# Kernel tuning notes

Measured on AMD Instinct MI355X. Metric: run time of the kernel, lower is better.

## Reference

```python
import jax, jax.numpy as jnp
import numpy as np

N, E, IN_CH, OUT_CH = 8192, 4096, 256, 256
EPS = 1e-06


def setup_inputs() -> dict:
    key = jax.random.key(0)
    k1, k2, k3, k4 = jax.random.split(key, 4)
    x = jax.random.normal(k1, (N, IN_CH), dtype=jnp.float32)
    H = jax.random.uniform(k2, (N, E), dtype=jnp.float32)
    # nn.Linear(in_ch, out_ch): weight [out_ch, in_ch], bias [out_ch]
    lim = 1.0 / np.sqrt(IN_CH)
    W = jax.random.uniform(k3, (OUT_CH, IN_CH), dtype=jnp.float32, minval=-lim, maxval=lim)
    b = jax.random.uniform(k4, (OUT_CH,), dtype=jnp.float32, minval=-lim, maxval=lim)
    return {"x": x, "H": H, "W": W, "b": b}


def reference(x, H, W, b):
    # A = Dv^{-1/2} H De^{-1} H^T Dv^{-1/2}; out = (A x) W^T + b
    d_e = H.sum(axis=0)                      # [E] hyperedge degrees
    d_v = H.sum(axis=1)                      # [N] node degrees
    de_inv = 1.0 / (d_e + EPS)               # [E]
    dv_is = (d_v + EPS) ** -0.5              # [N]
    # Diagonal matmuls expressed as row/col scaling (same math, no NxN/ExE diag GEMMs)
    xs = dv_is[:, None] * x                  # Dv^{-1/2} x            [N, C]
    t = de_inv[:, None] * (H.T @ xs)         # De^{-1} H^T (...)      [E, C]
    out = dv_is[:, None] * (H @ t)           # Dv^{-1/2} H (...)      [N, C]
    return out @ W.T + b
```

## Files before the change

kernel.cpp:

```cpp
#include <hip/hip_runtime.h>

#define NNODE 8192
#define NEDGE 4096
#define NCH   256
#define EPSV  1e-6f

typedef float  f32x4  __attribute__((ext_vector_type(4)));
typedef short  bf16x8 __attribute__((ext_vector_type(8)));
typedef unsigned short u16;
typedef unsigned int   u32;

static __device__ __forceinline__ u16 f2bf(float f) {
  union { float f; u32 u; } c; c.f = f;
  return (u16)((c.u + 0x7FFFu + ((c.u >> 16) & 1u)) >> 16);
}

static __device__ __forceinline__ void gload16(const u16* g, u16* l) {
  __builtin_amdgcn_global_load_lds((const __attribute__((address_space(1))) void*)g,
                                   (__attribute__((address_space(3))) void*)l,
                                   16, 0, 0);
}

static __device__ __forceinline__ uint4 pack8(const float4& a, const float4& c) {
  uint4 v;
  v.x = (u32)f2bf(a.x) | ((u32)f2bf(a.y) << 16);
  v.y = (u32)f2bf(a.z) | ((u32)f2bf(a.w) << 16);
  v.z = (u32)f2bf(c.x) | ((u32)f2bf(c.y) << 16);
  v.w = (u32)f2bf(c.z) | ((u32)f2bf(c.w) << 16);
  return v;
}

__global__ __launch_bounds__(256) void prep_h(const float* __restrict__ H,
                                              u16* __restrict__ HbT,
                                              float* __restrict__ d_v,
                                              float* __restrict__ d_e) {
  __shared__ float T[64][68];
  __shared__ float csp[16][68];
  __shared__ float rsum[64];
  const int t = threadIdx.x, a = t >> 4, b = t & 15;
  const int r0 = blockIdx.x * 64, c0 = blockIdx.y * 64;

  float4 v[4];
  #pragma unroll
  for (int i = 0; i < 4; ++i)
    v[i] = *(const float4*)&H[(size_t)(r0 + 4 * a + i) * NEDGE + c0 + 4 * b];

  #pragma unroll
  for (int i = 0; i < 4; ++i) {
    float rp = v[i].x + v[i].y + v[i].z + v[i].w;
    rp += __shfl_xor(rp, 1); rp += __shfl_xor(rp, 2);
    rp += __shfl_xor(rp, 4); rp += __shfl_xor(rp, 8);
    if (b == 0) rsum[4 * a + i] = rp;
  }
  csp[a][4 * b + 0] = v[0].x + v[1].x + v[2].x + v[3].x;
  csp[a][4 * b + 1] = v[0].y + v[1].y + v[2].y + v[3].y;
  csp[a][4 * b + 2] = v[0].z + v[1].z + v[2].z + v[3].z;
  csp[a][4 * b + 3] = v[0].w + v[1].w + v[2].w + v[3].w;

  {
    float4 w0 = {v[0].x, v[1].x, v[2].x, v[3].x};
    float4 w1 = {v[0].y, v[1].y, v[2].y, v[3].y};
    float4 w2 = {v[0].z, v[1].z, v[2].z, v[3].z};
    float4 w3 = {v[0].w, v[1].w, v[2].w, v[3].w};
    *(float4*)&T[4 * b + 0][4 * a] = w0;
    *(float4*)&T[4 * b + 1][4 * a] = w1;
    *(float4*)&T[4 * b + 2][4 * a] = w2;
    *(float4*)&T[4 * b + 3][4 * a] = w3;
  }
  __syncthreads();

  #pragma unroll
  for (int s = 0; s < 2; ++s) {
    const int idx = t + 256 * s;
    const int c = idx >> 3, g = idx & 7;
    const float4 p0 = *(const float4*)&T[c][8 * g];
    const float4 p1 = *(const float4*)&T[c][8 * g + 4];
    *(uint4*)&HbT[(size_t)(c0 + c) * NNODE + r0 + 8 * g] = pack8(p0, p1);
  }
  if (t < 64) {
    float s = 0.f;
    #pragma unroll
    for (int r = 0; r < 16; ++r) s += csp[r][t];
    atomicAdd(&d_e[c0 + t], s);
    atomicAdd(&d_v[r0 + t], rsum[t]);
  }
}

__global__ __launch_bounds__(256) void prep_x(const float* __restrict__ x,
                                              const float* __restrict__ d_v,
                                              u16* __restrict__ xsT) {
  __shared__ float T[64][68];
  const int t = threadIdx.x, a = t >> 4, b = t & 15;
  const int r0 = blockIdx.x * 64, c0 = blockIdx.y * 64;

  float4 v[4];
  #pragma unroll
  for (int i = 0; i < 4; ++i) {
    const int n = r0 + 4 * a + i;
    const float s = rsqrtf(d_v[n] + EPSV);
    float4 w = *(const float4*)&x[(size_t)n * NCH + c0 + 4 * b];
    w.x *= s; w.y *= s; w.z *= s; w.w *= s;
    v[i] = w;
  }
  {
    float4 w0 = {v[0].x, v[1].x, v[2].x, v[3].x};
    float4 w1 = {v[0].y, v[1].y, v[2].y, v[3].y};
    float4 w2 = {v[0].z, v[1].z, v[2].z, v[3].z};
    float4 w3 = {v[0].w, v[1].w, v[2].w, v[3].w};
    *(float4*)&T[4 * b + 0][4 * a] = w0;
    *(float4*)&T[4 * b + 1][4 * a] = w1;
    *(float4*)&T[4 * b + 2][4 * a] = w2;
    *(float4*)&T[4 * b + 3][4 * a] = w3;
  }
  __syncthreads();
  #pragma unroll
  for (int s = 0; s < 2; ++s) {
    const int idx = t + 256 * s;
    const int c = idx >> 3, g = idx & 7;
    const float4 p0 = *(const float4*)&T[c][8 * g];
    const float4 p1 = *(const float4*)&T[c][8 * g + 4];
    *(uint4*)&xsT[(size_t)(c0 + c) * NNODE + r0 + 8 * g] = pack8(p0, p1);
  }
}

__global__ __launch_bounds__(256) void prep_w(const float* __restrict__ W,
                                              u16* __restrict__ Wb) {
  const int i = (blockIdx.x * 256 + threadIdx.x) * 8;
  const float4 a = *(const float4*)&W[i];
  const float4 b = *(const float4*)&W[i + 4];
  *(uint4*)&Wb[i] = pack8(a, b);
}

__global__ __launch_bounds__(256) void init_out(const float* __restrict__ b,
                                                float* __restrict__ out) {
  const int i = (blockIdx.x * 256 + threadIdx.x) * 4;
  const float4 bb = *(const float4*)&b[i & 255];
  *(float4*)&out[i] = bb;
}

template <int ROWS, int NT>
static __device__ __forceinline__ void stage_gl(const u16* __restrict__ base,
                                                int row0, int K, int kt,
                                                u16* lds, int tid) {
  const int w = tid >> 6, l = tid & 63;
  #pragma unroll
  for (int i = 0; i < (ROWS * 8) / NT; ++i) {
    const int slot = i * NT + w * 64 + l;
    const int row = slot >> 3, ch = slot & 7;
    const int sch = ch ^ (row & 7);
    gload16(base + (size_t)(row0 + row) * K + kt + sch * 8,
            lds + (size_t)(i * NT + w * 64) * 8);
  }
}

template <int ROWS, int NT, int SCALE>
static __device__ __forceinline__ void stage_f32(const float* __restrict__ base,
                                                 int row0, int K, int kt,
                                                 const float* __restrict__ sv,
                                                 u16* lds, int tid) {
  for (int idx = tid; idx < ROWS * 8; idx += NT) {
    const int row = idx >> 3, ch = idx & 7;
    float s = 1.0f;
    if constexpr (SCALE == 1) s = 1.0f / (sv[row0 + row] + EPSV);
    const size_t g = (size_t)(row0 + row) * K + kt + ch * 8;
    float4 v0 = *(const float4*)&base[g];
    float4 v1 = *(const float4*)&base[g + 4];
    v0.x *= s; v0.y *= s; v0.z *= s; v0.w *= s;
    v1.x *= s; v1.y *= s; v1.z *= s; v1.w *= s;
    *(uint4*)&lds[row * 64 + ((ch ^ (row & 7)) * 8)] = pack8(v0, v1);
  }
}

template <int BM, int BN, int WM, int WN, int ASRC, int BSRC, int EPI>
__global__ __launch_bounds__(WM * WN * 64, 4) void gemm_nt(
    const void* __restrict__ Aptr, const void* __restrict__ Bptr,
    int K, int KC,
    const float* __restrict__ svb, const float* __restrict__ sve,
    void* __restrict__ Cout, int ldc) {
  constexpr int BK = 64;
  constexpr int NT = WM * WN * 64;
  constexpr int WMR = BM / WM, WNR = BN / WN;
  constexpr int FM = WMR / 16, FN = WNR / 16;
  __shared__ u16 lds_a[BM * BK];
  __shared__ u16 lds_b[BN * BK];

  const int tid  = threadIdx.x;
  const int lane = tid & 63;
  const int w    = tid >> 6;
  const int wm   = w / WN, wn = w % WN;
  const int m0   = blockIdx.x * BM;
  const int n0   = blockIdx.y * BN;
  const int k0   = blockIdx.z * KC;

  f32x4 acc[FM][FN];
  #pragma unroll
  for (int fm = 0; fm < FM; ++fm)
    #pragma unroll
    for (int fn = 0; fn < FN; ++fn)
      acc[fm][fn] = (f32x4){0.f, 0.f, 0.f, 0.f};

  for (int kt = k0; kt < k0 + KC; kt += BK) {
    __syncthreads();
    if constexpr (ASRC == 0) {
      stage_gl<BM, NT>((const u16*)Aptr, m0, K, kt, lds_a, tid);
    } else {
      stage_f32<BM, NT, 0>((const float*)Aptr, m0, K, kt, nullptr, lds_a, tid);
    }
    if constexpr (BSRC == 0) {
      stage_gl<BN, NT>((const u16*)Bptr, n0, K, kt, lds_b, tid);
    } else {
      stage_f32<BN, NT, 1>((const float*)Bptr, n0, K, kt, svb, lds_b, tid);
    }
    __syncthreads();

    #pragma unroll
    for (int kk = 0; kk < 2; ++kk) {
      bf16x8 af[FM], bfv[FN];
      #pragma unroll
      for (int fm = 0; fm < FM; ++fm) {
        const int row = wm * WMR + fm * 16 + (lane & 15);
        const int ch  = kk * 4 + (lane >> 4);
        af[fm] = *(const bf16x8*)&lds_a[row * BK + ((ch ^ (row & 7)) * 8)];
      }
      #pragma unroll
      for (int fn = 0; fn < FN; ++fn) {
        const int row = wn * WNR + fn * 16 + (lane & 15);
        const int ch  = kk * 4 + (lane >> 4);
        bfv[fn] = *(const bf16x8*)&lds_b[row * BK + ((ch ^ (row & 7)) * 8)];
      }
      #pragma unroll
      for (int fm = 0; fm < FM; ++fm)
        #pragma unroll
        for (int fn = 0; fn < FN; ++fn)
          acc[fm][fn] = __builtin_amdgcn_mfma_f32_16x16x32_bf16(
              af[fm], bfv[fn], acc[fm][fn], 0, 0, 0);
    }
  }

  if constexpr (EPI == 0) {
    float* C = (float*)Cout;
    #pragma unroll
    for (int fm = 0; fm < FM; ++fm) {
      const int rowb = m0 + wm * WMR + fm * 16 + ((lane >> 4) << 2);
      #pragma unroll
      for (int fn = 0; fn < FN; ++fn) {
        const int col = n0 + wn * WNR + fn * 16 + (lane & 15);
        #pragma unroll
        for (int r = 0; r < 4; ++r)
          atomicAdd(&C[(size_t)(rowb + r) * ldc + col], acc[fm][fn][r]);
      }
    }
  } else if constexpr (EPI == 1) {
    float* C = (float*)Cout;
    #pragma unroll
    for (int fm = 0; fm < FM; ++fm) {
      const int rowb = m0 + wm * WMR + fm * 16 + ((lane >> 4) << 2);
      float s[4];
      #pragma unroll
      for (int r = 0; r < 4; ++r) s[r] = rsqrtf(sve[rowb + r] + EPSV);
      #pragma unroll
      for (int fn = 0; fn < FN; ++fn) {
        const int col = n0 + wn * WNR + fn * 16 + (lane & 15);
        #pragma unroll
        for (int r = 0; r < 4; ++r)
          atomicAdd(&C[(size_t)(rowb + r) * ldc + col], acc[fm][fn][r] * s[r]);
      }
    }
  } else {
    u16* C = (u16*)Cout;
    #pragma unroll
    for (int fm = 0; fm < FM; ++fm) {
      const int rowb = m0 + wm * WMR + fm * 16 + ((lane >> 4) << 2);
      #pragma unroll
      for (int fn = 0; fn < FN; ++fn) {
        const int col = n0 + wn * WNR + fn * 16 + (lane & 15);
        #pragma unroll
        for (int r = 0; r < 4; ++r)
          C[(size_t)(rowb + r) * ldc + col] = f2bf(acc[fm][fn][r]);
      }
    }
  }
}

extern "C" void kernel_launch(void* const* d_in, const int* in_sizes, int n_in,
                              void* d_out, int out_size, void* d_ws, size_t ws_size,
                              hipStream_t stream) {
  const float* x = (const float*)d_in[0];
  const float* H = (const float*)d_in[1];
  const float* W = (const float*)d_in[2];
  const float* b = (const float*)d_in[3];
  float* out = (float*)d_out;

  char* ws = (char*)d_ws;
  u16*   HbT  = (u16*)(ws);
  u16*   xsT  = (u16*)(ws + 67108864ull);
  float* tAcc = (float*)(ws + 71303168ull);
  u16*   uT   = (u16*)(ws + 75497472ull);
  u16*   Wb   = (u16*)(ws + 77594624ull);
  float* dv   = (float*)(ws + 77725696ull);
  float* de   = (float*)(ws + 77758464ull);

  hipMemsetAsync(dv, 0, (NNODE + NEDGE) * sizeof(float), stream);
  hipMemsetAsync(tAcc, 0, (size_t)NEDGE * NCH * sizeof(float), stream);

  prep_h<<<dim3(NNODE / 64, NEDGE / 64), 256, 0, stream>>>(H, HbT, dv, de);
  prep_x<<<dim3(NNODE / 64, NCH / 64), 256, 0, stream>>>(x, dv, xsT);
  prep_w<<<32, 256, 0, stream>>>(W, Wb);
  init_out<<<(NNODE * NCH) / 1024, 256, 0, stream>>>(b, out);

  gemm_nt<128, 256, 2, 4, 0, 0, 0><<<dim3(NEDGE / 128, 1, 16), 512, 0, stream>>>(
      HbT, xsT, NNODE, NNODE / 16, nullptr, nullptr, tAcc, NCH);
  gemm_nt<64, 64, 2, 2, 0, 1, 2><<<dim3(4, NEDGE / 64, 1), 256, 0, stream>>>(
      Wb, tAcc, NCH, NCH, de, nullptr, uT, NEDGE);
  gemm_nt<128, 256, 2, 4, 1, 0, 1><<<dim3(NNODE / 128, 1, 8), 512, 0, stream>>>(
      H, uT, NEDGE, NEDGE / 8, nullptr, dv, out, NCH);
}
```

Before: 379.2 us.

## Replace atomic split-K accumulation with partial buffers and fused reduction kernels

The split-K GEMMs now write fp32 partial results to separate slices instead of using atomicAdd into a zeroed buffer. Two new reduce kernels sum the 8 slices and apply the scaling: de^-1 with a bf16 pack for t, and dv^-1/2 plus bias for the output. The middle GEMM now reads a pre-packed bf16 t, so it no longer needs an fp32 staging path. This removes the tAcc memset, the init_out kernel and atomic contention, at the cost of extra partial-buffer traffic (8 slices of NxC fp32 for the output, about 64MB) and two more launches.

```diff
diff --git a/kernel.cpp b/kernel.cpp
--- a/kernel.cpp
+++ b/kernel.cpp
@@ -131,11 +131,51 @@
   *(uint4*)&Wb[i] = pack8(a, b);
 }
 
-__global__ __launch_bounds__(256) void init_out(const float* __restrict__ b,
-                                                float* __restrict__ out) {
-  const int i = (blockIdx.x * 256 + threadIdx.x) * 4;
-  const float4 bb = *(const float4*)&b[i & 255];
-  *(float4*)&out[i] = bb;
+__global__ __launch_bounds__(256) void reduce1(const float* __restrict__ tPart,
+                                               const float* __restrict__ de,
+                                               u16* __restrict__ t) {
+  const int base = (blockIdx.x * 256 + threadIdx.x) * 8;
+  const int e = base >> 8;
+  float4 s0 = {0.f, 0.f, 0.f, 0.f}, s1 = {0.f, 0.f, 0.f, 0.f};
+  #pragma unroll
+  for (int s = 0; s < 8; ++s) {
+    const float* p = tPart + (size_t)s * (NEDGE * NCH) + base;
+    const float4 a = *(const float4*)p;
+    const float4 c = *(const float4*)(p + 4);
+    s0.x += a.x; s0.y += a.y; s0.z += a.z; s0.w += a.w;
+    s1.x += c.x; s1.y += c.y; s1.z += c.z; s1.w += c.w;
+  }
+  const float inv = 1.0f / (de[e] + EPSV);
+  s0.x *= inv; s0.y *= inv; s0.z *= inv; s0.w *= inv;
+  s1.x *= inv; s1.y *= inv; s1.z *= inv; s1.w *= inv;
+  *(uint4*)&t[base] = pack8(s0, s1);
+}
+
+__global__ __launch_bounds__(256) void reduce2(const float* __restrict__ oPart,
+                                               const float* __restrict__ dv,
+                                               const float* __restrict__ b,
+                                               float* __restrict__ out) {
+  const int base = (blockIdx.x * 256 + threadIdx.x) * 8;
+  const int n = base >> 8, o0 = base & 255;
+  float4 s0 = {0.f, 0.f, 0.f, 0.f}, s1 = {0.f, 0.f, 0.f, 0.f};
+  #pragma unroll
+  for (int s = 0; s < 8; ++s) {
+    const float* p = oPart + (size_t)s * (NNODE * NCH) + base;
+    const float4 a = *(const float4*)p;
+    const float4 c = *(const float4*)(p + 4);
+    s0.x += a.x; s0.y += a.y; s0.z += a.z; s0.w += a.w;
+    s1.x += c.x; s1.y += c.y; s1.z += c.z; s1.w += c.w;
+  }
+  const float sc = rsqrtf(dv[n] + EPSV);
+  const float4 b0 = *(const float4*)&b[o0];
+  const float4 b1 = *(const float4*)&b[o0 + 4];
+  float4 r0, r1;
+  r0.x = s0.x * sc + b0.x; r0.y = s0.y * sc + b0.y;
+  r0.z = s0.z * sc + b0.z; r0.w = s0.w * sc + b0.w;
+  r1.x = s1.x * sc + b1.x; r1.y = s1.y * sc + b1.y;
+  r1.z = s1.z * sc + b1.z; r1.w = s1.w * sc + b1.w;
+  *(float4*)&out[base] = r0;
+  *(float4*)&out[base + 4] = r1;
 }
 
 template <int ROWS, int NT>
@@ -153,30 +193,26 @@
   }
 }
 
-template <int ROWS, int NT, int SCALE>
+template <int ROWS, int NT>
 static __device__ __forceinline__ void stage_f32(const float* __restrict__ base,
                                                  int row0, int K, int kt,
-                                                 const float* __restrict__ sv,
                                                  u16* lds, int tid) {
-  for (int idx = tid; idx < ROWS * 8; idx += NT) {
+  #pragma unroll
+  for (int i = 0; i < (ROWS * 8) / NT; ++i) {
+    const int idx = i * NT + tid;
     const int row = idx >> 3, ch = idx & 7;
-    float s = 1.0f;
-    if constexpr (SCALE == 1) s = 1.0f / (sv[row0 + row] + EPSV);
     const size_t g = (size_t)(row0 + row) * K + kt + ch * 8;
-    float4 v0 = *(const float4*)&base[g];
-    float4 v1 = *(const float4*)&base[g + 4];
-    v0.x *= s; v0.y *= s; v0.z *= s; v0.w *= s;
-    v1.x *= s; v1.y *= s; v1.z *= s; v1.w *= s;
+    const float4 v0 = *(const float4*)&base[g];
+    const float4 v1 = *(const float4*)&base[g + 4];
     *(uint4*)&lds[row * 64 + ((ch ^ (row & 7)) * 8)] = pack8(v0, v1);
   }
 }
 
-template <int BM, int BN, int WM, int WN, int ASRC, int BSRC, int EPI>
+template <int BM, int BN, int WM, int WN, int ASRC, int EPI>
 __global__ __launch_bounds__(WM * WN * 64, 4) void gemm_nt(
-    const void* __restrict__ Aptr, const void* __restrict__ Bptr,
+    const void* __restrict__ Aptr, const u16* __restrict__ Bt,
     int K, int KC,
-    const float* __restrict__ svb, const float* __restrict__ sve,
-    void* __restrict__ Cout, int ldc) {
+    void* __restrict__ Cout, int ldc, size_t pstride) {
   constexpr int BK = 64;
   constexpr int NT = WM * WN * 64;
   constexpr int WMR = BM / WM, WNR = BN / WN;
@@ -204,13 +240,9 @@
     if constexpr (ASRC == 0) {
       stage_gl<BM, NT>((const u16*)Aptr, m0, K, kt, lds_a, tid);
     } else {
-      stage_f32<BM, NT, 0>((const float*)Aptr, m0, K, kt, nullptr, lds_a, tid);
+      stage_f32<BM, NT>((const float*)Aptr, m0, K, kt, lds_a, tid);
     }
-    if constexpr (BSRC == 0) {
-      stage_gl<BN, NT>((const u16*)Bptr, n0, K, kt, lds_b, tid);
-    } else {
-      stage_f32<BN, NT, 1>((const float*)Bptr, n0, K, kt, svb, lds_b, tid);
-    }
+    stage_gl<BN, NT>(Bt, n0, K, kt, lds_b, tid);
     __syncthreads();
 
     #pragma unroll
@@ -238,7 +270,7 @@
   }
 
   if constexpr (EPI == 0) {
-    float* C = (float*)Cout;
+    float* C = (float*)Cout + (size_t)blockIdx.z * pstride;
     #pragma unroll
     for (int fm = 0; fm < FM; ++fm) {
       const int rowb = m0 + wm * WMR + fm * 16 + ((lane >> 4) << 2);
@@ -247,23 +279,7 @@
         const int col = n0 + wn * WNR + fn * 16 + (lane & 15);
         #pragma unroll
         for (int r = 0; r < 4; ++r)
-          atomicAdd(&C[(size_t)(rowb + r) * ldc + col], acc[fm][fn][r]);
-      }
-    }
-  } else if constexpr (EPI == 1) {
-    float* C = (float*)Cout;
-    #pragma unroll
-    for (int fm = 0; fm < FM; ++fm) {
-      const int rowb = m0 + wm * WMR + fm * 16 + ((lane >> 4) << 2);
-      float s[4];
-      #pragma unroll
-      for (int r = 0; r < 4; ++r) s[r] = rsqrtf(sve[rowb + r] + EPSV);
-      #pragma unroll
-      for (int fn = 0; fn < FN; ++fn) {
-        const int col = n0 + wn * WNR + fn * 16 + (lane & 15);
-        #pragma unroll
-        for (int r = 0; r < 4; ++r)
-          atomicAdd(&C[(size_t)(rowb + r) * ldc + col], acc[fm][fn][r] * s[r]);
+          C[(size_t)(rowb + r) * ldc + col] = acc[fm][fn][r];
       }
     }
   } else {
@@ -292,26 +308,28 @@
   float* out = (float*)d_out;
 
   char* ws = (char*)d_ws;
-  u16*   HbT  = (u16*)(ws);
-  u16*   xsT  = (u16*)(ws + 67108864ull);
-  float* tAcc = (float*)(ws + 71303168ull);
-  u16*   uT   = (u16*)(ws + 75497472ull);
-  u16*   Wb   = (u16*)(ws + 77594624ull);
-  float* dv   = (float*)(ws + 77725696ull);
-  float* de   = (float*)(ws + 77758464ull);
+  u16*   HbT   = (u16*)(ws);
+  u16*   xsT   = (u16*)(ws + 67108864ull);
+  u16*   t     = (u16*)(ws + 71303168ull);
+  u16*   uT    = (u16*)(ws + 73400320ull);
+  u16*   Wb    = (u16*)(ws + 75497472ull);
+  float* dv    = (float*)(ws + 75628544ull);
+  float* de    = (float*)(ws + 75661312ull);
+  float* tPart = (float*)(ws + 75694080ull);
+  float* oPart = (float*)(ws + 75694080ull);
 
   hipMemsetAsync(dv, 0, (NNODE + NEDGE) * sizeof(float), stream);
-  hipMemsetAsync(tAcc, 0, (size_t)NEDGE * NCH * sizeof(float), stream);
 
   prep_h<<<dim3(NNODE / 64, NEDGE / 64), 256, 0, stream>>>(H, HbT, dv, de);
   prep_x<<<dim3(NNODE / 64, NCH / 64), 256, 0, stream>>>(x, dv, xsT);
   prep_w<<<32, 256, 0, stream>>>(W, Wb);
-  init_out<<<(NNODE * NCH) / 1024, 256, 0, stream>>>(b, out);
-
-  gemm_nt<128, 256, 2, 4, 0, 0, 0><<<dim3(NEDGE / 128, 1, 16), 512, 0, stream>>>(
-      HbT, xsT, NNODE, NNODE / 16, nullptr, nullptr, tAcc, NCH);
-  gemm_nt<64, 64, 2, 2, 0, 1, 2><<<dim3(4, NEDGE / 64, 1), 256, 0, stream>>>(
-      Wb, tAcc, NCH, NCH, de, nullptr, uT, NEDGE);
-  gemm_nt<128, 256, 2, 4, 1, 0, 1><<<dim3(NNODE / 128, 1, 8), 512, 0, stream>>>(
-      H, uT, NEDGE, NEDGE / 8, nullptr, dv, out, NCH);
-}
+
+  gemm_nt<128, 128, 2, 2, 0, 0><<<dim3(NEDGE / 128, NCH / 128, 8), 256, 0, stream>>>(
+      HbT, xsT, NNODE, NNODE / 8, tPart, NCH, (size_t)NEDGE * NCH);
+  reduce1<<<(NEDGE * NCH) / 2048, 256, 0, stream>>>(tPart, de, t);
+  gemm_nt<128, 128, 2, 2, 0, 2><<<dim3(NCH / 128, NEDGE / 128, 1), 256, 0, stream>>>(
+      Wb, t, NCH, NCH, uT, NEDGE, 0);
+  gemm_nt<128, 256, 2, 4, 1, 0><<<dim3(NNODE / 128, 1, 8), 512, 0, stream>>>(
+      H, uT, NEDGE, NEDGE / 8, oPart, NCH, (size_t)NNODE * NCH);
+  reduce2<<<(NNODE * NCH) / 2048, 256, 0, stream>>>(oPart, dv, b, out);
+}
```

Result: faster. 315.6 us (-16.8%).
